# Kernel tuning notes

Hardware: AMD Instinct MI355X
Metric: run time of the kernel (lower is better)

## Reference

```python
import jax, jax.numpy as jnp
import numpy as np

N = 50000
E = 800000
IN_C = 128
HID = 128
HID2 = 256
OUT_C = 40


def setup_inputs() -> dict:
    key = jax.random.key(0)
    ks = jax.random.split(key, 12)
    x = jax.random.normal(ks[0], (N, IN_C), dtype=jnp.float32)
    edge_index = jax.random.randint(ks[1], (2, E), 0, N, dtype=jnp.int64)
    def lin(k, fi, fo):
        # torch Linear default init: U(-1/sqrt(fi), 1/sqrt(fi))
        b = 1.0 / np.sqrt(fi)
        k1, k2 = jax.random.split(k)
        W = jax.random.uniform(k1, (fi, fo), minval=-b, maxval=b, dtype=jnp.float32)
        bvec = jax.random.uniform(k2, (fo,), minval=-b, maxval=b, dtype=jnp.float32)
        return W, bvec
    W1, b1 = lin(ks[2], IN_C, HID)
    W2, b2 = lin(ks[3], HID, HID)
    W3, b3 = lin(ks[4], HID, HID2)
    W4, b4 = lin(ks[5], HID2, HID2)
    Wl, bl = lin(ks[6], HID2, OUT_C)
    return {"x": x, "edge_index": edge_index,
            "W1": W1, "b1": b1, "W2": W2, "b2": b2,
            "W3": W3, "b3": b3, "W4": W4, "b4": b4,
            "Wl": Wl, "bl": bl}


def gin_conv(x, src, dst, Wa, ba, Wb, bb):
    # GINConv, eps=0: h_i = MLP(x_i + sum_{j->i} x_j)
    agg = jax.ops.segment_sum(x[src], dst, num_segments=N)  # [N, d]
    h = x + agg
    h = jax.nn.relu(h @ Wa + ba)
    return h @ Wb + bb


def reference(x, edge_index, W1, b1, W2, b2, W3, b3, W4, b4, Wl, bl):
    src, dst = edge_index[0], edge_index[1]
    h = jax.nn.relu(gin_conv(x, src, dst, W1, b1, W2, b2))
    # dropout p=0.5 is identity in eval mode
    h = jax.nn.relu(gin_conv(h, src, dst, W3, b3, W4, b4))
    return h @ Wl + bl
```

## Files before the change

kernel.cpp:

```cpp
#include <hip/hip_runtime.h>
#include <hip/hip_bf16.h>
#include <hip/hip_fp16.h>
#include <stdint.h>

#define N_NODES 50000
#define E_EDGES 800000
#define NBKT 196
#define PBUF 6144

typedef short s16x8 __attribute__((ext_vector_type(8)));
typedef _Float16 f16x8 __attribute__((ext_vector_type(8)));
typedef float f32x4 __attribute__((ext_vector_type(4)));

__device__ __forceinline__ unsigned short f2h_bits(float f) {
    return __half_as_ushort(__float2half(f));
}
__device__ __forceinline__ float h2f(unsigned short u) {
    __half h = *reinterpret_cast<const __half*>(&u);
    return __half2float(h);
}
__device__ __forceinline__ float2 h2f2(unsigned int u) {
    __half2 h = *reinterpret_cast<const __half2*>(&u);
    return __half22float2(h);
}

__global__ __launch_bounds__(256) void khist_conv(
    const int* __restrict__ dst, int* __restrict__ gbcnt,
    const float* __restrict__ x, unsigned short* __restrict__ xh) {
    __shared__ int bcnt[NBKT];
    int t = threadIdx.x;
    for (int i = t; i < NBKT; i += 256) bcnt[i] = 0;
    __syncthreads();
    int gid = blockIdx.x * 256 + t;
    const int STRIDE = 256 * 256;
    const float4* xv = (const float4*)x;
    for (int e = gid; e < E_EDGES; e += STRIDE) {
        atomicAdd(&bcnt[dst[e] >> 8], 1);
        float4 a = xv[(size_t)2 * e];
        float4 b = xv[(size_t)2 * e + 1];
        s16x8 h;
        h[0] = (short)f2h_bits(a.x); h[1] = (short)f2h_bits(a.y);
        h[2] = (short)f2h_bits(a.z); h[3] = (short)f2h_bits(a.w);
        h[4] = (short)f2h_bits(b.x); h[5] = (short)f2h_bits(b.y);
        h[6] = (short)f2h_bits(b.z); h[7] = (short)f2h_bits(b.w);
        *(s16x8*)(xh + (size_t)e * 8) = h;
    }
    __syncthreads();
    for (int i = t; i < NBKT; i += 256) atomicAdd(&gbcnt[i], bcnt[i]);
}

__global__ void scan_bkt(const int* __restrict__ gbcnt, int* __restrict__ bscan,
                         int* __restrict__ gcur) {
    __shared__ int wsum[4];
    int t = threadIdx.x, lane = t & 63, wid = t >> 6;
    int v = (t < NBKT) ? gbcnt[t] : 0;
    int x = v;
#pragma unroll
    for (int off = 1; off < 64; off <<= 1) {
        int tt = __shfl_up(x, off);
        if (lane >= off) x += tt;
    }
    if (lane == 63) wsum[wid] = x;
    __syncthreads();
    if (t == 0) {
        int s = 0;
#pragma unroll
        for (int i = 0; i < 4; i++) { int tmp = wsum[i]; wsum[i] = s; s += tmp; }
    }
    __syncthreads();
    int excl = x - v + wsum[wid];
    if (t <= NBKT) bscan[t] = excl;
    if (t < NBKT) gcur[t] = excl;
}

__global__ __launch_bounds__(256) void bin_pass(
    const int* __restrict__ src, const int* __restrict__ dst,
    int* __restrict__ gcur, unsigned int* __restrict__ pool) {
    __shared__ unsigned int lbuf[NBKT][64];
    __shared__ int lcnt[NBKT];
    __shared__ int lbase[NBKT];
    int tid = threadIdx.x;
    for (int i = tid; i < NBKT; i += 256) lcnt[i] = 0;
    __syncthreads();
    const int EPG = (E_EDGES + gridDim.x - 1) / gridDim.x;
    int e0 = blockIdx.x * EPG;
    int e1 = e0 + EPG; if (e1 > E_EDGES) e1 = E_EDGES;
    for (int wbase = e0; wbase < e1; wbase += 2048) {
        int wend = wbase + 2048; if (wend > e1) wend = e1;
        int d8[8], s8[8], n8 = 0;
        {
            int e = wbase + tid;
#pragma unroll
            for (int k = 0; k < 8; k++, e += 256)
                if (e < wend) { d8[n8] = dst[e]; s8[n8] = src[e]; n8++; }
        }
        for (int k = 0; k < n8; k++) {
            int d = d8[k];
            unsigned int rec = (unsigned int)(s8[k] & 0xFFFF) |
                               ((unsigned int)(d & 255) << 16);
            int b = d >> 8;
            int slot = atomicAdd(&lcnt[b], 1);
            if (slot < 64) lbuf[b][slot] = rec;
            else pool[atomicAdd(&gcur[b], 1)] = rec;
        }
        __syncthreads();
        if (tid < NBKT) {
            int c = lcnt[tid]; if (c > 64) c = 64;
            int lines = c >> 5;
            if (lines) lbase[tid] = atomicAdd(&gcur[tid], lines * 32);
        }
        __syncthreads();
        {
            int wid = tid >> 6, lane = tid & 63;
            for (int b = wid * 49; b < (wid + 1) * 49; b++) {
                int c = lcnt[b]; if (c > 64) c = 64;
                int lines = c >> 5, rem = c & 31;
                for (int l = 0; l < lines; l++)
                    if (lane < 32)
                        pool[lbase[b] + l * 32 + lane] = lbuf[b][l * 32 + lane];
                if (lines && lane < rem) lbuf[b][lane] = lbuf[b][lines * 32 + lane];
                if (lane == 0) lcnt[b] = rem;
            }
        }
        __syncthreads();
    }
    if (tid < NBKT) {
        int c = lcnt[tid]; if (c > 64) c = 64;
        if (c) lbase[tid] = atomicAdd(&gcur[tid], c);
    }
    __syncthreads();
    {
        int wid = tid >> 6, lane = tid & 63;
        for (int b = wid * 49; b < (wid + 1) * 49; b++) {
            int c = lcnt[b]; if (c > 64) c = 64;
            if (lane < c) pool[lbase[b] + lane] = lbuf[b][lane];
        }
    }
}

__global__ __launch_bounds__(256) void build_csr(
    const unsigned int* __restrict__ pool, const int* __restrict__ bscan,
    int* __restrict__ rowptr, unsigned short* __restrict__ perm) {
    __shared__ int ncnt[256];
    __shared__ int ncur[256];
    __shared__ int wsum[4];
    __shared__ unsigned short pbuf[PBUF];
    int b = blockIdx.x, t = threadIdx.x;
    int base = bscan[b], K = bscan[b + 1] - base;
    ncnt[t] = 0;
    __syncthreads();
    for (int i = t; i < K; i += 256)
        atomicAdd(&ncnt[(pool[base + i] >> 16) & 255], 1);
    __syncthreads();
    int lane = t & 63, wid = t >> 6;
    int v = ncnt[t], x = v;
#pragma unroll
    for (int off = 1; off < 64; off <<= 1) {
        int tt = __shfl_up(x, off);
        if (lane >= off) x += tt;
    }
    if (lane == 63) wsum[wid] = x;
    __syncthreads();
    if (t == 0) {
        int s = 0;
#pragma unroll
        for (int i = 0; i < 4; i++) { int tmp = wsum[i]; wsum[i] = s; s += tmp; }
    }
    __syncthreads();
    int excl = x - v + wsum[wid];
    int node = b * 256 + t;
    if (node <= N_NODES) rowptr[node] = base + excl;
    ncur[t] = excl;
    __syncthreads();
    for (int i = t; i < K; i += 256) {
        unsigned int rec = pool[base + i];
        int nl = (rec >> 16) & 255;
        int pos = atomicAdd(&ncur[nl], 1);
        if (pos < PBUF) pbuf[pos] = (unsigned short)rec;
        else perm[base + pos] = (unsigned short)rec;
    }
    __syncthreads();
    int KK = K < PBUF ? K : PBUF;
    for (int i = t; i < KK; i += 256) perm[base + i] = pbuf[i];
}

__global__ __launch_bounds__(256) void gather_agg_h(
    const unsigned short* __restrict__ feat,
    const int* __restrict__ rowptr,
    const unsigned short* __restrict__ perm,
    unsigned short* __restrict__ out) {
    int node = (blockIdx.x * 256 + threadIdx.x) >> 6;
    if (node >= N_NODES) return;
    int lane = threadIdx.x & 63;
    int sub = lane >> 4;
    int c4 = lane & 15;
    const uint4* fv = (const uint4*)feat;
    float acc[8];
    {
        uint4 sv = fv[(size_t)node * 16 + c4];
        float2 a0 = h2f2(sv.x), a1 = h2f2(sv.y), a2 = h2f2(sv.z), a3 = h2f2(sv.w);
        float m = (sub == 0) ? 1.f : 0.f;
        acc[0] = m * a0.x; acc[1] = m * a0.y;
        acc[2] = m * a1.x; acc[3] = m * a1.y;
        acc[4] = m * a2.x; acc[5] = m * a2.y;
        acc[6] = m * a3.x; acc[7] = m * a3.y;
    }
    int beg = rowptr[node], end = rowptr[node + 1];
    for (int base = beg; base < end; base += 64) {
        int cnt = end - base; if (cnt > 64) cnt = 64;
        int pv = (base + lane < end) ? (int)perm[base + lane] : 0;
        int j = 0;
        for (; j + 15 < cnt; j += 16) {
            int s0 = __shfl(pv, j + sub);
            int s1 = __shfl(pv, j + 4 + sub);
            int s2 = __shfl(pv, j + 8 + sub);
            int s3 = __shfl(pv, j + 12 + sub);
            uint4 u0 = fv[(size_t)s0 * 16 + c4];
            uint4 u1 = fv[(size_t)s1 * 16 + c4];
            uint4 u2 = fv[(size_t)s2 * 16 + c4];
            uint4 u3 = fv[(size_t)s3 * 16 + c4];
#pragma unroll
            for (int k = 0; k < 4; k++) {
                uint4 u = k == 0 ? u0 : (k == 1 ? u1 : (k == 2 ? u2 : u3));
                float2 a0 = h2f2(u.x), a1 = h2f2(u.y), a2 = h2f2(u.z), a3 = h2f2(u.w);
                acc[0] += a0.x; acc[1] += a0.y;
                acc[2] += a1.x; acc[3] += a1.y;
                acc[4] += a2.x; acc[5] += a2.y;
                acc[6] += a3.x; acc[7] += a3.y;
            }
        }
        for (; j + 3 < cnt; j += 4) {
            int s = __shfl(pv, j + sub);
            uint4 u = fv[(size_t)s * 16 + c4];
            float2 a0 = h2f2(u.x), a1 = h2f2(u.y), a2 = h2f2(u.z), a3 = h2f2(u.w);
            acc[0] += a0.x; acc[1] += a0.y;
            acc[2] += a1.x; acc[3] += a1.y;
            acc[4] += a2.x; acc[5] += a2.y;
            acc[6] += a3.x; acc[7] += a3.y;
        }
        if (j < cnt) {
            int ix = j + sub;
            bool ok = ix < cnt;
            int s = __shfl(pv, ok ? ix : j);
            uint4 u = fv[(size_t)s * 16 + c4];
            float m = ok ? 1.f : 0.f;
            float2 a0 = h2f2(u.x), a1 = h2f2(u.y), a2 = h2f2(u.z), a3 = h2f2(u.w);
            acc[0] += m * a0.x; acc[1] += m * a0.y;
            acc[2] += m * a1.x; acc[3] += m * a1.y;
            acc[4] += m * a2.x; acc[5] += m * a2.y;
            acc[6] += m * a3.x; acc[7] += m * a3.y;
        }
    }
#pragma unroll
    for (int i = 0; i < 8; i++) {
        acc[i] += __shfl_xor(acc[i], 16);
        acc[i] += __shfl_xor(acc[i], 32);
    }
    if (sub == 0) {
        uint4 o;
        o.x = (unsigned int)f2h_bits(acc[0]) | ((unsigned int)f2h_bits(acc[1]) << 16);
        o.y = (unsigned int)f2h_bits(acc[2]) | ((unsigned int)f2h_bits(acc[3]) << 16);
        o.z = (unsigned int)f2h_bits(acc[4]) | ((unsigned int)f2h_bits(acc[5]) << 16);
        o.w = (unsigned int)f2h_bits(acc[6]) | ((unsigned int)f2h_bits(acc[7]) << 16);
        ((uint4*)out)[(size_t)node * 16 + c4] = o;
    }
}

__device__ __forceinline__ void prep_one(const float* __restrict__ W,
                                         unsigned short* __restrict__ Whi,
                                         int K, int F, int Fpad, int i) {
    int S = K / 32, T = Fpad / 16;
    int total = T * S * 64;
    if (i >= total) return;
    int lane = i & 63;
    int s = (i >> 6) % S;
    int t = (i >> 6) / S;
    int col = t * 16 + (lane & 15);
    int k0 = s * 32 + (lane >> 4) * 8;
    s16x8 vh;
#pragma unroll
    for (int j = 0; j < 8; j++) {
        float w = (col < F) ? W[(size_t)(k0 + j) * F + col] : 0.f;
        vh[j] = (short)f2h_bits(w);
    }
    *(s16x8*)(Whi + (size_t)i * 8) = vh;
}

__global__ void prep_all(const float* W1, const float* W2, const float* W3,
                         const float* W4, const float* Wl,
                         unsigned short* W1h, unsigned short* W2h,
                         unsigned short* W3h, unsigned short* W4h,
                         unsigned short* Wlh) {
    int b = blockIdx.x, t = threadIdx.x;
    if (b < 8)       prep_one(W1, W1h, 128, 128, 128, b * 256 + t);
    else if (b < 16) prep_one(W2, W2h, 128, 128, 128, (b - 8) * 256 + t);
    else if (b < 32) prep_one(W3, W3h, 128, 256, 256, (b - 16) * 256 + t);
    else if (b < 64) prep_one(W4, W4h, 256, 256, 256, (b - 32) * 256 + t);
    else             prep_one(Wl, Wlh, 256, 40, 64, (b - 64) * 256 + t);
}

__device__ __forceinline__ void lds_store_h(unsigned short* lds, int C,
                                            int row, int col, unsigned short v) {
    int cb = col >> 3, e = col & 7;
    lds[row * C + (((cb ^ row) & (C / 8 - 1)) << 3) + e] = v;
}
__device__ __forceinline__ f16x8 lds_load_frag(const unsigned short* lds, int C,
                                               int row, int cb) {
    return *(const f16x8*)(lds + row * C + (((cb ^ row) & (C / 8 - 1)) << 3));
}

__global__ __launch_bounds__(256) void layer1_mlp(
    const unsigned short* __restrict__ A,
    const unsigned short* __restrict__ W1h, const float* __restrict__ b1,
    const unsigned short* __restrict__ W2h, const float* __restrict__ b2,
    unsigned short* __restrict__ out) {
    __shared__ unsigned short h1[32 * 128];
    const int wave = threadIdx.x >> 6, lane = threadIdx.x & 63;
    const int lm = lane & 15, quad = lane >> 4;
    const int row0 = blockIdx.x * 32;
    bool rv1 = (row0 + 16) < N_NODES;

    {
        f16x8 a[2][4];
#pragma unroll
        for (int r = 0; r < 2; r++) {
            int rr = (r == 0 || rv1) ? row0 + r * 16 : row0;
            const unsigned short* ap = A + (size_t)(rr + lm) * 128 + quad * 8;
#pragma unroll
            for (int s = 0; s < 4; s++) a[r][s] = *(const f16x8*)(ap + s * 32);
        }
        f32x4 acc[2][2];
#pragma unroll
        for (int t = 0; t < 2; t++)
#pragma unroll
            for (int r = 0; r < 2; r++) {
                f32x4 z = {0.f, 0.f, 0.f, 0.f};
                acc[t][r] = z;
            }
#pragma unroll
        for (int s = 0; s < 4; s++) {
#pragma unroll
            for (int t = 0; t < 2; t++) {
                int tg = wave * 2 + t;
                const f16x8 bh = *(const f16x8*)(W1h + (size_t)((tg * 4 + s) * 64 + lane) * 8);
#pragma unroll
                for (int r = 0; r < 2; r++)
                    acc[t][r] = __builtin_amdgcn_mfma_f32_16x16x32_f16(a[r][s], bh, acc[t][r], 0, 0, 0);
            }
        }
#pragma unroll
        for (int r = 0; r < 2; r++)
#pragma unroll
            for (int t = 0; t < 2; t++) {
                int col = (wave * 2 + t) * 16 + lm;
                float bv = b1[col];
#pragma unroll
                for (int q = 0; q < 4; q++) {
                    float vv = fmaxf(acc[t][r][q] + bv, 0.f);
                    lds_store_h(h1, 128, r * 16 + quad * 4 + q, col, f2h_bits(vv));
                }
            }
    }
    __syncthreads();

    {
        f32x4 acc[2][2];
#pragma unroll
        for (int t = 0; t < 2; t++)
#pragma unroll
            for (int r = 0; r < 2; r++) {
                f32x4 z = {0.f, 0.f, 0.f, 0.f};
                acc[t][r] = z;
            }
#pragma unroll
        for (int s = 0; s < 4; s++) {
            f16x8 a0 = lds_load_frag(h1, 128, lm, s * 4 + quad);
            f16x8 a1 = lds_load_frag(h1, 128, 16 + lm, s * 4 + quad);
#pragma unroll
            for (int t = 0; t < 2; t++) {
                int tg = wave * 2 + t;
                const f16x8 bh = *(const f16x8*)(W2h + (size_t)((tg * 4 + s) * 64 + lane) * 8);
                acc[t][0] = __builtin_amdgcn_mfma_f32_16x16x32_f16(a0, bh, acc[t][0], 0, 0, 0);
                acc[t][1] = __builtin_amdgcn_mfma_f32_16x16x32_f16(a1, bh, acc[t][1], 0, 0, 0);
            }
        }
#pragma unroll
        for (int r = 0; r < 2; r++) {
            if (r == 1 && !rv1) break;
            int orow = row0 + r * 16 + quad * 4;
#pragma unroll
            for (int t = 0; t < 2; t++) {
                int col = (wave * 2 + t) * 16 + lm;
                float bv = b2[col];
#pragma unroll
                for (int q = 0; q < 4; q++) {
                    float vv = fmaxf(acc[t][r][q] + bv, 0.f);
                    out[(size_t)(orow + q) * 128 + col] = f2h_bits(vv);
                }
            }
        }
    }
}

__global__ __launch_bounds__(256) void layer2_mlp(
    const unsigned short* __restrict__ A,
    const unsigned short* __restrict__ W3h, const float* __restrict__ b3,
    const unsigned short* __restrict__ W4h, const float* __restrict__ b4,
    const unsigned short* __restrict__ Wlh, const float* __restrict__ bl,
    float* __restrict__ out) {
    __shared__ unsigned short h2[32 * 256];
    __shared__ unsigned short h2b[32 * 256];
    const int wave = threadIdx.x >> 6, lane = threadIdx.x & 63;
    const int lm = lane & 15, quad = lane >> 4;
    const int row0 = blockIdx.x * 32;
    bool rv1 = (row0 + 16) < N_NODES;

    {
        f16x8 a[2][4];
#pragma unroll
        for (int r = 0; r < 2; r++) {
            int rr = (r == 0 || rv1) ? row0 + r * 16 : row0;
            const unsigned short* ap = A + (size_t)(rr + lm) * 128 + quad * 8;
#pragma unroll
            for (int s = 0; s < 4; s++) a[r][s] = *(const f16x8*)(ap + s * 32);
        }
        f32x4 acc[4][2];
#pragma unroll
        for (int t = 0; t < 4; t++)
#pragma unroll
            for (int r = 0; r < 2; r++) {
                f32x4 z = {0.f, 0.f, 0.f, 0.f};
                acc[t][r] = z;
            }
#pragma unroll
        for (int s = 0; s < 4; s++) {
#pragma unroll
            for (int t = 0; t < 4; t++) {
                int tg = wave * 4 + t;
                const f16x8 bh = *(const f16x8*)(W3h + (size_t)((tg * 4 + s) * 64 + lane) * 8);
#pragma unroll
                for (int r = 0; r < 2; r++)
                    acc[t][r] = __builtin_amdgcn_mfma_f32_16x16x32_f16(a[r][s], bh, acc[t][r], 0, 0, 0);
            }
        }
#pragma unroll
        for (int r = 0; r < 2; r++)
#pragma unroll
            for (int t = 0; t < 4; t++) {
                int col = (wave * 4 + t) * 16 + lm;
                float bv = b3[col];
#pragma unroll
                for (int q = 0; q < 4; q++) {
                    float vv = fmaxf(acc[t][r][q] + bv, 0.f);
                    lds_store_h(h2, 256, r * 16 + quad * 4 + q, col, f2h_bits(vv));
                }
            }
    }
    __syncthreads();

    {
        f32x4 acc[4][2];
#pragma unroll
        for (int t = 0; t < 4; t++)
#pragma unroll
            for (int r = 0; r < 2; r++) {
                f32x4 z = {0.f, 0.f, 0.f, 0.f};
                acc[t][r] = z;
            }
#pragma unroll
        for (int s = 0; s < 8; s++) {
            f16x8 a0 = lds_load_frag(h2, 256, lm, s * 4 + quad);
            f16x8 a1 = lds_load_frag(h2, 256, 16 + lm, s * 4 + quad);
#pragma unroll
            for (int t = 0; t < 4; t++) {
                int tg = wave * 4 + t;
                const f16x8 bh = *(const f16x8*)(W4h + (size_t)((tg * 8 + s) * 64 + lane) * 8);
                acc[t][0] = __builtin_amdgcn_mfma_f32_16x16x32_f16(a0, bh, acc[t][0], 0, 0, 0);
                acc[t][1] = __builtin_amdgcn_mfma_f32_16x16x32_f16(a1, bh, acc[t][1], 0, 0, 0);
            }
        }
        __syncthreads();
#pragma unroll
        for (int r = 0; r < 2; r++)
#pragma unroll
            for (int t = 0; t < 4; t++) {
                int col = (wave * 4 + t) * 16 + lm;
                float bv = b4[col];
#pragma unroll
                for (int q = 0; q < 4; q++) {
                    float vv = fmaxf(acc[t][r][q] + bv, 0.f);
                    lds_store_h(h2b, 256, r * 16 + quad * 4 + q, col, f2h_bits(vv));
                }
            }
    }
    __syncthreads();

    {
        f32x4 acc[2];
        {
            f32x4 z = {0.f, 0.f, 0.f, 0.f};
            acc[0] = z; acc[1] = z;
        }
#pragma unroll
        for (int s = 0; s < 8; s++) {
            f16x8 a0 = lds_load_frag(h2b, 256, lm, s * 4 + quad);
            f16x8 a1 = lds_load_frag(h2b, 256, 16 + lm, s * 4 + quad);
            const f16x8 bh = *(const f16x8*)(Wlh + (size_t)((wave * 8 + s) * 64 + lane) * 8);
            acc[0] = __builtin_amdgcn_mfma_f32_16x16x32_f16(a0, bh, acc[0], 0, 0, 0);
            acc[1] = __builtin_amdgcn_mfma_f32_16x16x32_f16(a1, bh, acc[1], 0, 0, 0);
        }
        int col = wave * 16 + lm;
        if (col < 40) {
            float bv = bl[col];
#pragma unroll
            for (int r = 0; r < 2; r++) {
                if (r == 1 && !rv1) break;
                int orow = row0 + r * 16 + quad * 4;
#pragma unroll
                for (int q = 0; q < 4; q++) {
                    out[(size_t)(orow + q) * 40 + col] = acc[r][q] + bv;
                }
            }
        }
    }
}

extern "C" void kernel_launch(void* const* d_in, const int* in_sizes, int n_in,
                              void* d_out, int out_size, void* d_ws, size_t ws_size,
                              hipStream_t stream) {
    const float* x  = (const float*)d_in[0];
    const int* ei   = (const int*)d_in[1];
    const float* W1 = (const float*)d_in[2];
    const float* b1 = (const float*)d_in[3];
    const float* W2 = (const float*)d_in[4];
    const float* b2 = (const float*)d_in[5];
    const float* W3 = (const float*)d_in[6];
    const float* b3 = (const float*)d_in[7];
    const float* W4 = (const float*)d_in[8];
    const float* b4 = (const float*)d_in[9];
    const float* Wl = (const float*)d_in[10];
    const float* bl = (const float*)d_in[11];
    float* out = (float*)d_out;

    const int* src = ei;
    const int* dst = ei + E_EDGES;

    char* ws = (char*)d_ws;
    size_t off = 0;
    unsigned short* xh  = (unsigned short*)(ws + off); off += (size_t)N_NODES * 128 * 2;
    unsigned short* hFh = (unsigned short*)(ws + off); off += (size_t)N_NODES * 128 * 2;
    unsigned short* W1h = (unsigned short*)(ws + off); off += 16384 * 2;
    unsigned short* W2h = (unsigned short*)(ws + off); off += 16384 * 2;
    unsigned short* W3h = (unsigned short*)(ws + off); off += 32768 * 2;
    unsigned short* W4h = (unsigned short*)(ws + off); off += 65536 * 2;
    unsigned short* Wlh = (unsigned short*)(ws + off); off += 16384 * 2;
    off = (off + 255) & ~(size_t)255;
    unsigned int* pool = (unsigned int*)(ws + off); off += (size_t)E_EDGES * 4;
    unsigned short* perm = (unsigned short*)(ws + off); off += (size_t)E_EDGES * 2;
    off = (off + 255) & ~(size_t)255;
    int* rowptr = (int*)(ws + off); off += (size_t)(N_NODES + 1) * 4;
    int* gbcnt  = (int*)(ws + off); off += 256 * 4;
    int* bscan  = (int*)(ws + off); off += 256 * 4;
    int* gcur   = (int*)(ws + off); off += 256 * 4;
    (void)ws_size; (void)in_sizes; (void)n_in; (void)out_size;

    (void)hipMemsetAsync(gbcnt, 0, 256 * 4, stream);
    khist_conv<<<256, 256, 0, stream>>>(dst, gbcnt, x, xh);
    scan_bkt<<<1, 256, 0, stream>>>(gbcnt, bscan, gcur);
    bin_pass<<<256, 256, 0, stream>>>(src, dst, gcur, pool);
    build_csr<<<NBKT, 256, 0, stream>>>(pool, bscan, rowptr, perm);

    prep_all<<<72, 256, 0, stream>>>(W1, W2, W3, W4, Wl,
                                     W1h, W2h, W3h, W4h, Wlh);

    const int aggBlocks = (N_NODES * 64 + 255) / 256;
    const int rblk = (N_NODES + 31) / 32;

    gather_agg_h<<<aggBlocks, 256, 0, stream>>>(xh, rowptr, perm, hFh);
    layer1_mlp<<<rblk, 256, 0, stream>>>(hFh, W1h, b1, W2h, b2, xh);

    gather_agg_h<<<aggBlocks, 256, 0, stream>>>(xh, rowptr, perm, hFh);
    layer2_mlp<<<rblk, 256, 0, stream>>>(hFh, W3h, b3, W4h, b4, Wlh, bl, out);
}
```

Measured before the change: 262.5 us.

## Fuse neighbor gather-aggregation into MLP kernels via LDS staging

Removes the standalone gather_agg_h kernels and performs the neighbor sum inside each layer's MLP kernel, writing the aggregated 32-row tile into swizzled LDS, from which the MFMA A-fragments are loaded. This drops two kernel launches and the write and re-read of the intermediate aggregated feature buffer in global memory. In exchange, each wave now gathers 8 nodes sequentially inside the MLP block, and the extra LDS may lower occupancy during the latency-bound gather phase. Layer 1 output now goes to a separate buffer instead of overwriting the input.

```diff
diff --git a/kernel.cpp b/kernel.cpp
--- a/kernel.cpp
+++ b/kernel.cpp
@@ -184,88 +184,6 @@
     for (int i = t; i < KK; i += 256) perm[base + i] = pbuf[i];
 }
 
-__global__ __launch_bounds__(256) void gather_agg_h(
-    const unsigned short* __restrict__ feat,
-    const int* __restrict__ rowptr,
-    const unsigned short* __restrict__ perm,
-    unsigned short* __restrict__ out) {
-    int node = (blockIdx.x * 256 + threadIdx.x) >> 6;
-    if (node >= N_NODES) return;
-    int lane = threadIdx.x & 63;
-    int sub = lane >> 4;
-    int c4 = lane & 15;
-    const uint4* fv = (const uint4*)feat;
-    float acc[8];
-    {
-        uint4 sv = fv[(size_t)node * 16 + c4];
-        float2 a0 = h2f2(sv.x), a1 = h2f2(sv.y), a2 = h2f2(sv.z), a3 = h2f2(sv.w);
-        float m = (sub == 0) ? 1.f : 0.f;
-        acc[0] = m * a0.x; acc[1] = m * a0.y;
-        acc[2] = m * a1.x; acc[3] = m * a1.y;
-        acc[4] = m * a2.x; acc[5] = m * a2.y;
-        acc[6] = m * a3.x; acc[7] = m * a3.y;
-    }
-    int beg = rowptr[node], end = rowptr[node + 1];
-    for (int base = beg; base < end; base += 64) {
-        int cnt = end - base; if (cnt > 64) cnt = 64;
-        int pv = (base + lane < end) ? (int)perm[base + lane] : 0;
-        int j = 0;
-        for (; j + 15 < cnt; j += 16) {
-            int s0 = __shfl(pv, j + sub);
-            int s1 = __shfl(pv, j + 4 + sub);
-            int s2 = __shfl(pv, j + 8 + sub);
-            int s3 = __shfl(pv, j + 12 + sub);
-            uint4 u0 = fv[(size_t)s0 * 16 + c4];
-            uint4 u1 = fv[(size_t)s1 * 16 + c4];
-            uint4 u2 = fv[(size_t)s2 * 16 + c4];
-            uint4 u3 = fv[(size_t)s3 * 16 + c4];
-#pragma unroll
-            for (int k = 0; k < 4; k++) {
-                uint4 u = k == 0 ? u0 : (k == 1 ? u1 : (k == 2 ? u2 : u3));
-                float2 a0 = h2f2(u.x), a1 = h2f2(u.y), a2 = h2f2(u.z), a3 = h2f2(u.w);
-                acc[0] += a0.x; acc[1] += a0.y;
-                acc[2] += a1.x; acc[3] += a1.y;
-                acc[4] += a2.x; acc[5] += a2.y;
-                acc[6] += a3.x; acc[7] += a3.y;
-            }
-        }
-        for (; j + 3 < cnt; j += 4) {
-            int s = __shfl(pv, j + sub);
-            uint4 u = fv[(size_t)s * 16 + c4];
-            float2 a0 = h2f2(u.x), a1 = h2f2(u.y), a2 = h2f2(u.z), a3 = h2f2(u.w);
-            acc[0] += a0.x; acc[1] += a0.y;
-            acc[2] += a1.x; acc[3] += a1.y;
-            acc[4] += a2.x; acc[5] += a2.y;
-            acc[6] += a3.x; acc[7] += a3.y;
-        }
-        if (j < cnt) {
-            int ix = j + sub;
-            bool ok = ix < cnt;
-            int s = __shfl(pv, ok ? ix : j);
-            uint4 u = fv[(size_t)s * 16 + c4];
-            float m = ok ? 1.f : 0.f;
-            float2 a0 = h2f2(u.x), a1 = h2f2(u.y), a2 = h2f2(u.z), a3 = h2f2(u.w);
-            acc[0] += m * a0.x; acc[1] += m * a0.y;
-            acc[2] += m * a1.x; acc[3] += m * a1.y;
-            acc[4] += m * a2.x; acc[5] += m * a2.y;
-            acc[6] += m * a3.x; acc[7] += m * a3.y;
-        }
-    }
-#pragma unroll
-    for (int i = 0; i < 8; i++) {
-        acc[i] += __shfl_xor(acc[i], 16);
-        acc[i] += __shfl_xor(acc[i], 32);
-    }
-    if (sub == 0) {
-        uint4 o;
-        o.x = (unsigned int)f2h_bits(acc[0]) | ((unsigned int)f2h_bits(acc[1]) << 16);
-        o.y = (unsigned int)f2h_bits(acc[2]) | ((unsigned int)f2h_bits(acc[3]) << 16);
-        o.z = (unsigned int)f2h_bits(acc[4]) | ((unsigned int)f2h_bits(acc[5]) << 16);
-        o.w = (unsigned int)f2h_bits(acc[6]) | ((unsigned int)f2h_bits(acc[7]) << 16);
-        ((uint4*)out)[(size_t)node * 16 + c4] = o;
-    }
-}
-
 __device__ __forceinline__ void prep_one(const float* __restrict__ W,
                                          unsigned short* __restrict__ Whi,
                                          int K, int F, int Fpad, int i) {
@@ -299,6 +217,7 @@
     else             prep_one(Wl, Wlh, 256, 40, 64, (b - 64) * 256 + t);
 }
 
+
 __device__ __forceinline__ void lds_store_h(unsigned short* lds, int C,
                                             int row, int col, unsigned short v) {
     int cb = col >> 3, e = col & 7;
@@ -309,26 +228,109 @@
     return *(const f16x8*)(lds + row * C + (((cb ^ row) & (C / 8 - 1)) << 3));
 }
 
-__global__ __launch_bounds__(256) void layer1_mlp(
-    const unsigned short* __restrict__ A,
+__device__ __forceinline__ void gather_to_lds(
+    const unsigned short* __restrict__ feat,
+    const int* __restrict__ rowptr,
+    const unsigned short* __restrict__ perm,
+    unsigned short* Albuf, int row0, int wave, int lane) {
+    int sub = lane >> 4, c4 = lane & 15;
+    const uint4* fv = (const uint4*)feat;
+#pragma unroll 1
+    for (int i = 0; i < 8; i++) {
+        int lrow = wave * 8 + i;
+        int node = row0 + lrow;
+        float acc[8];
+        if (node < N_NODES) {
+            uint4 sv = fv[(size_t)node * 16 + c4];
+            float2 a0 = h2f2(sv.x), a1 = h2f2(sv.y), a2 = h2f2(sv.z), a3 = h2f2(sv.w);
+            float m = (sub == 0) ? 1.f : 0.f;
+            acc[0] = m * a0.x; acc[1] = m * a0.y;
+            acc[2] = m * a1.x; acc[3] = m * a1.y;
+            acc[4] = m * a2.x; acc[5] = m * a2.y;
+            acc[6] = m * a3.x; acc[7] = m * a3.y;
+            int beg = rowptr[node], end = rowptr[node + 1];
+            for (int base = beg; base < end; base += 64) {
+                int cnt = end - base; if (cnt > 64) cnt = 64;
+                int pv = (base + lane < end) ? (int)perm[base + lane] : 0;
+                int j = 0;
+                for (; j + 15 < cnt; j += 16) {
+                    int s0 = __shfl(pv, j + sub);
+                    int s1 = __shfl(pv, j + 4 + sub);
+                    int s2 = __shfl(pv, j + 8 + sub);
+                    int s3 = __shfl(pv, j + 12 + sub);
+                    uint4 u0 = fv[(size_t)s0 * 16 + c4];
+                    uint4 u1 = fv[(size_t)s1 * 16 + c4];
+                    uint4 u2 = fv[(size_t)s2 * 16 + c4];
+                    uint4 u3 = fv[(size_t)s3 * 16 + c4];
+#pragma unroll
+                    for (int k = 0; k < 4; k++) {
+                        uint4 u = k == 0 ? u0 : (k == 1 ? u1 : (k == 2 ? u2 : u3));
+                        float2 b0 = h2f2(u.x), b1 = h2f2(u.y), b2 = h2f2(u.z), b3 = h2f2(u.w);
+                        acc[0] += b0.x; acc[1] += b0.y;
+                        acc[2] += b1.x; acc[3] += b1.y;
+                        acc[4] += b2.x; acc[5] += b2.y;
+                        acc[6] += b3.x; acc[7] += b3.y;
+                    }
+                }
+                for (; j + 3 < cnt; j += 4) {
+                    int s = __shfl(pv, j + sub);
+                    uint4 u = fv[(size_t)s * 16 + c4];
+                    float2 b0 = h2f2(u.x), b1 = h2f2(u.y), b2 = h2f2(u.z), b3 = h2f2(u.w);
+                    acc[0] += b0.x; acc[1] += b0.y;
+                    acc[2] += b1.x; acc[3] += b1.y;
+                    acc[4] += b2.x; acc[5] += b2.y;
+                    acc[6] += b3.x; acc[7] += b3.y;
+                }
+                if (j < cnt) {
+                    int ix = j + sub;
+                    bool ok = ix < cnt;
+                    int s = __shfl(pv, ok ? ix : j);
+                    uint4 u = fv[(size_t)s * 16 + c4];
+                    float m2 = ok ? 1.f : 0.f;
+                    float2 b0 = h2f2(u.x), b1 = h2f2(u.y), b2 = h2f2(u.z), b3 = h2f2(u.w);
+                    acc[0] += m2 * b0.x; acc[1] += m2 * b0.y;
+                    acc[2] += m2 * b1.x; acc[3] += m2 * b1.y;
+                    acc[4] += m2 * b2.x; acc[5] += m2 * b2.y;
+                    acc[6] += m2 * b3.x; acc[7] += m2 * b3.y;
+                }
+            }
+#pragma unroll
+            for (int k = 0; k < 8; k++) {
+                acc[k] += __shfl_xor(acc[k], 16);
+                acc[k] += __shfl_xor(acc[k], 32);
+            }
+        } else {
+#pragma unroll
+            for (int k = 0; k < 8; k++) acc[k] = 0.f;
+        }
+        if (sub == 0) {
+            uint4 o;
+            o.x = (unsigned int)f2h_bits(acc[0]) | ((unsigned int)f2h_bits(acc[1]) << 16);
+            o.y = (unsigned int)f2h_bits(acc[2]) | ((unsigned int)f2h_bits(acc[3]) << 16);
+            o.z = (unsigned int)f2h_bits(acc[4]) | ((unsigned int)f2h_bits(acc[5]) << 16);
+            o.w = (unsigned int)f2h_bits(acc[6]) | ((unsigned int)f2h_bits(acc[7]) << 16);
+            ((uint4*)(Albuf + lrow * 128))[(c4 ^ lrow) & 15] = o;
+        }
+    }
+}
+
+__global__ __launch_bounds__(256) void fused_layer1(
+    const unsigned short* __restrict__ feat,
+    const int* __restrict__ rowptr, const unsigned short* __restrict__ perm,
     const unsigned short* __restrict__ W1h, const float* __restrict__ b1,
     const unsigned short* __restrict__ W2h, const float* __restrict__ b2,
     unsigned short* __restrict__ out) {
+    __shared__ unsigned short Albuf[32 * 128];
     __shared__ unsigned short h1[32 * 128];
     const int wave = threadIdx.x >> 6, lane = threadIdx.x & 63;
     const int lm = lane & 15, quad = lane >> 4;
     const int row0 = blockIdx.x * 32;
     bool rv1 = (row0 + 16) < N_NODES;
 
+    gather_to_lds(feat, rowptr, perm, Albuf, row0, wave, lane);
+    __syncthreads();
+
     {
-        f16x8 a[2][4];
-#pragma unroll
-        for (int r = 0; r < 2; r++) {
-            int rr = (r == 0 || rv1) ? row0 + r * 16 : row0;
-            const unsigned short* ap = A + (size_t)(rr + lm) * 128 + quad * 8;
-#pragma unroll
-            for (int s = 0; s < 4; s++) a[r][s] = *(const f16x8*)(ap + s * 32);
-        }
         f32x4 acc[2][2];
 #pragma unroll
         for (int t = 0; t < 2; t++)
@@ -339,13 +341,14 @@
             }
 #pragma unroll
         for (int s = 0; s < 4; s++) {
+            f16x8 a0 = lds_load_frag(Albuf, 128, lm, s * 4 + quad);
+            f16x8 a1 = lds_load_frag(Albuf, 128, 16 + lm, s * 4 + quad);
 #pragma unroll
             for (int t = 0; t < 2; t++) {
                 int tg = wave * 2 + t;
                 const f16x8 bh = *(const f16x8*)(W1h + (size_t)((tg * 4 + s) * 64 + lane) * 8);
-#pragma unroll
-                for (int r = 0; r < 2; r++)
-                    acc[t][r] = __builtin_amdgcn_mfma_f32_16x16x32_f16(a[r][s], bh, acc[t][r], 0, 0, 0);
+                acc[t][0] = __builtin_amdgcn_mfma_f32_16x16x32_f16(a0, bh, acc[t][0], 0, 0, 0);
+                acc[t][1] = __builtin_amdgcn_mfma_f32_16x16x32_f16(a1, bh, acc[t][1], 0, 0, 0);
             }
         }
 #pragma unroll
@@ -402,12 +405,14 @@
     }
 }
 
-__global__ __launch_bounds__(256) void layer2_mlp(
-    const unsigned short* __restrict__ A,
+__global__ __launch_bounds__(256) void fused_layer2(
+    const unsigned short* __restrict__ feat,
+    const int* __restrict__ rowptr, const unsigned short* __restrict__ perm,
     const unsigned short* __restrict__ W3h, const float* __restrict__ b3,
     const unsigned short* __restrict__ W4h, const float* __restrict__ b4,
     const unsigned short* __restrict__ Wlh, const float* __restrict__ bl,
     float* __restrict__ out) {
+    __shared__ unsigned short Albuf[32 * 128];
     __shared__ unsigned short h2[32 * 256];
     __shared__ unsigned short h2b[32 * 256];
     const int wave = threadIdx.x >> 6, lane = threadIdx.x & 63;
@@ -415,15 +420,10 @@
     const int row0 = blockIdx.x * 32;
     bool rv1 = (row0 + 16) < N_NODES;
 
+    gather_to_lds(feat, rowptr, perm, Albuf, row0, wave, lane);
+    __syncthreads();
+
     {
-        f16x8 a[2][4];
-#pragma unroll
-        for (int r = 0; r < 2; r++) {
-            int rr = (r == 0 || rv1) ? row0 + r * 16 : row0;
-            const unsigned short* ap = A + (size_t)(rr + lm) * 128 + quad * 8;
-#pragma unroll
-            for (int s = 0; s < 4; s++) a[r][s] = *(const f16x8*)(ap + s * 32);
-        }
         f32x4 acc[4][2];
 #pragma unroll
         for (int t = 0; t < 4; t++)
@@ -434,13 +434,14 @@
             }
 #pragma unroll
         for (int s = 0; s < 4; s++) {
+            f16x8 a0 = lds_load_frag(Albuf, 128, lm, s * 4 + quad);
+            f16x8 a1 = lds_load_frag(Albuf, 128, 16 + lm, s * 4 + quad);
 #pragma unroll
             for (int t = 0; t < 4; t++) {
                 int tg = wave * 4 + t;
                 const f16x8 bh = *(const f16x8*)(W3h + (size_t)((tg * 4 + s) * 64 + lane) * 8);
-#pragma unroll
-                for (int r = 0; r < 2; r++)
-                    acc[t][r] = __builtin_amdgcn_mfma_f32_16x16x32_f16(a[r][s], bh, acc[t][r], 0, 0, 0);
+                acc[t][0] = __builtin_amdgcn_mfma_f32_16x16x32_f16(a0, bh, acc[t][0], 0, 0, 0);
+                acc[t][1] = __builtin_amdgcn_mfma_f32_16x16x32_f16(a1, bh, acc[t][1], 0, 0, 0);
             }
         }
 #pragma unroll
@@ -548,7 +549,7 @@
     char* ws = (char*)d_ws;
     size_t off = 0;
     unsigned short* xh  = (unsigned short*)(ws + off); off += (size_t)N_NODES * 128 * 2;
-    unsigned short* hFh = (unsigned short*)(ws + off); off += (size_t)N_NODES * 128 * 2;
+    unsigned short* xh2 = (unsigned short*)(ws + off); off += (size_t)N_NODES * 128 * 2;
     unsigned short* W1h = (unsigned short*)(ws + off); off += 16384 * 2;
     unsigned short* W2h = (unsigned short*)(ws + off); off += 16384 * 2;
     unsigned short* W3h = (unsigned short*)(ws + off); off += 32768 * 2;
@@ -573,12 +574,11 @@
     prep_all<<<72, 256, 0, stream>>>(W1, W2, W3, W4, Wl,
                                      W1h, W2h, W3h, W4h, Wlh);
 
-    const int aggBlocks = (N_NODES * 64 + 255) / 256;
     const int rblk = (N_NODES + 31) / 32;
 
-    gather_agg_h<<<aggBlocks, 256, 0, stream>>>(xh, rowptr, perm, hFh);
-    layer1_mlp<<<rblk, 256, 0, stream>>>(hFh, W1h, b1, W2h, b2, xh);
-
-    gather_agg_h<<<aggBlocks, 256, 0, stream>>>(xh, rowptr, perm, hFh);
-    layer2_mlp<<<rblk, 256, 0, stream>>>(hFh, W3h, b3, W4h, b4, Wlh, bl, out);
-}
+    fused_layer1<<<rblk, 256, 0, stream>>>(xh, rowptr, perm,
+                                           W1h, b1, W2h, b2, xh2);
+
+    fused_layer2<<<rblk, 256, 0, stream>>>(xh2, rowptr, perm,
+                                           W3h, b3, W4h, b4, Wlh, bl, out);
+}
```

Result: slower. 298.3 us (+13.6%).
